# Performance work log

Measured on AMD Instinct MI355X. Metric: run time of the kernel, lower is better.

Reference implementation:

```python
import jax, jax.numpy as jnp
import numpy as np

BOS_TAG_ID = 0
EOS_TAG_ID = 1
NB_FEATURES = 5_000_000
T, L, F_PER = 16384, 64, 14


def setup_inputs() -> dict:
    key = jax.random.key(0)
    k1, k2, k3 = jax.random.split(key, 3)
    feat_idx = jax.random.randint(k1, (T, L, F_PER), 0, NB_FEATURES, dtype=jnp.int64 if jax.config.jax_enable_x64 else jnp.int32)
    emission_weights = jax.random.normal(k2, (NB_FEATURES, 1), dtype=jnp.float32)
    transitions = jax.random.normal(k3, (L, L), dtype=jnp.float32)
    return {"feat_idx": feat_idx, "emission_weights": emission_weights, "transitions": transitions}


def _get_emissions(feat_idx, emission_weights):
    # sparse [L, F] one-hot-count matrix @ [F,1] == gather + sum over the 14 feature ids
    w = emission_weights[:, 0]
    return w[feat_idx].sum(-1)[None]  # [1, T, L]


def _viterbi(emissions, transitions):
    B, T_, L_ = emissions.shape
    alpha0 = transitions[BOS_TAG_ID][None, :] + emissions[:, 0]  # [B, L]

    def step(alpha, em_t):
        # scores[b, prev, cur] = em_t[b, cur] + transitions[prev, cur] + alpha[b, prev]
        scores = em_t[:, None, :] + transitions[None] + alpha[:, :, None]
        new_alpha = scores.max(axis=1)
        bp = scores.argmax(axis=1)  # [B, L]
        return new_alpha, bp

    em_rest = jnp.swapaxes(emissions[:, 1:], 0, 1)  # [T-1, B, L]
    alpha, bps = jax.lax.scan(step, alpha0, em_rest)
    end_scores = alpha + transitions[:, EOS_TAG_ID][None, :]
    max_final_scores = end_scores.max(axis=1)
    final_tags = end_scores.argmax(axis=1)  # [B]

    def back(tag, bp):
        prev = jnp.take_along_axis(bp, tag[:, None], axis=1)[:, 0]
        return prev, prev

    _, path_rest = jax.lax.scan(back, final_tags, bps, reverse=True)  # [T-1, B]
    path = jnp.concatenate([path_rest.T, final_tags[:, None]], axis=1)  # [B, T]
    return max_final_scores, path


def reference(feat_idx, emission_weights, transitions):
    emissions = _get_emissions(feat_idx, emission_weights)
    scores, path = _viterbi(emissions, transitions)
    return scores, path
```

## Files before the change

kernel.cpp:

```cpp
#include <hip/hip_runtime.h>

#define T_LEN  16384
#define LTAG   64
#define F_PER  14
#define NCHUNK 1024
#define CHUNK  16
#define BOS_ID 0
#define EOS_ID 1
#define NREG   6
#define REGSZ  833334
#define WARM   48
#define WB     96

typedef __attribute__((ext_vector_type(4))) int i4;

static constexpr size_t EM_OFF = 0;
static constexpr size_t BP_OFF = EM_OFF + (size_t)T_LEN * 64 * 4;
static constexpr size_t AE_OFF = BP_OFF + (size_t)T_LEN * 64;
static constexpr size_t PS_OFF = AE_OFF + 512;

__global__ __launch_bounds__(256) void k_emissions(
    const int* __restrict__ idx, const float* __restrict__ w, float* __restrict__ em)
{
    __shared__ int sIdx[256 * F_PER];
    const int tid = threadIdx.x;
    const int* g = idx + (size_t)blockIdx.x * (256 * F_PER);
    for (int x = tid * 4; x < 256 * F_PER; x += 1024)
        *(i4*)(sIdx + x) = __builtin_nontemporal_load((const i4*)(g + x));
    __syncthreads();
    int id[F_PER];
#pragma unroll
    for (int f = 0; f < F_PER; ++f) id[f] = sIdx[tid * F_PER + f];
    float sf[F_PER];
#pragma unroll
    for (int f = 0; f < F_PER; ++f) sf[f] = 0.f;
    for (int r = 0; r < NREG; ++r) {
        const int lo = r * REGSZ;
#pragma unroll
        for (int f = 0; f < F_PER; ++f)
            if ((unsigned)(id[f] - lo) < (unsigned)REGSZ) sf[f] += w[id[f]];
    }
    float s = 0.f;
#pragma unroll
    for (int f = 0; f < F_PER; f += 2) s += sf[f] + sf[f + 1];
    em[(size_t)blockIdx.x * 256 + tid] = s;
}

__global__ __launch_bounds__(64, 1) void k_phase3(
    const float* __restrict__ trans, const float* __restrict__ em,
    unsigned char* __restrict__ bp, float* __restrict__ aEnd)
{
    __shared__ __align__(16) float sa[64];
    const int c = blockIdx.x;
    const int tid = threadIdx.x;
    const int t0 = c * CHUNK;
    int nsteps = (T_LEN - 1) - t0; if (nsteps > CHUNK) nsteps = CHUNK;

    float tr_[64];
#pragma unroll
    for (int i = 0; i < 64; ++i) tr_[i] = trans[i * 64 + tid];

    float a; int tw;
    if (t0 <= WARM) { tw = 0; a = tr_[BOS_ID] + em[tid]; }
    else            { tw = t0 - WARM; a = em[(size_t)tw * 64 + tid]; }

    float e_nxt = em[(size_t)(tw + 1) * 64 + tid];
    const float4* ap = (const float4*)sa;

    for (int t = tw + 1; t <= t0; ++t) {
        const float e = e_nxt;
        e_nxt = em[(size_t)(t + 1) * 64 + tid];
        sa[tid] = a;
        float m = -3.0e38f;
#pragma unroll
        for (int g = 0; g < 4; ++g) {
            const float4 v0 = ap[4*g+0], v1 = ap[4*g+1], v2 = ap[4*g+2], v3 = ap[4*g+3];
            float s0[16];
            s0[0]  = tr_[16*g+0]  + v0.x;  s0[1]  = tr_[16*g+1]  + v0.y;
            s0[2]  = tr_[16*g+2]  + v0.z;  s0[3]  = tr_[16*g+3]  + v0.w;
            s0[4]  = tr_[16*g+4]  + v1.x;  s0[5]  = tr_[16*g+5]  + v1.y;
            s0[6]  = tr_[16*g+6]  + v1.z;  s0[7]  = tr_[16*g+7]  + v1.w;
            s0[8]  = tr_[16*g+8]  + v2.x;  s0[9]  = tr_[16*g+9]  + v2.y;
            s0[10] = tr_[16*g+10] + v2.z;  s0[11] = tr_[16*g+11] + v2.w;
            s0[12] = tr_[16*g+12] + v3.x;  s0[13] = tr_[16*g+13] + v3.y;
            s0[14] = tr_[16*g+14] + v3.z;  s0[15] = tr_[16*g+15] + v3.w;
#pragma unroll
            for (int st = 8; st >= 1; st >>= 1)
#pragma unroll
                for (int i = 0; i < st; ++i) s0[i] = fmaxf(s0[i], s0[i + st]);
            m = fmaxf(m, s0[0]);
        }
        a = e + m;
    }

    const int tend = t0 + nsteps;
    for (int t = t0 + 1; t <= tend; ++t) {
        const float e = e_nxt;
        const int tn = (t + 1 <= T_LEN - 1) ? t + 1 : T_LEN - 1;
        e_nxt = em[(size_t)tn * 64 + tid];
        sa[tid] = a;
        float m = -3.0e38f; int bi = 0;
#pragma unroll
        for (int g = 0; g < 4; ++g) {
            const float4 v0 = ap[4*g+0], v1 = ap[4*g+1], v2 = ap[4*g+2], v3 = ap[4*g+3];
            float s0[16];
            s0[0]  = tr_[16*g+0]  + v0.x;  s0[1]  = tr_[16*g+1]  + v0.y;
            s0[2]  = tr_[16*g+2]  + v0.z;  s0[3]  = tr_[16*g+3]  + v0.w;
            s0[4]  = tr_[16*g+4]  + v1.x;  s0[5]  = tr_[16*g+5]  + v1.y;
            s0[6]  = tr_[16*g+6]  + v1.z;  s0[7]  = tr_[16*g+7]  + v1.w;
            s0[8]  = tr_[16*g+8]  + v2.x;  s0[9]  = tr_[16*g+9]  + v2.y;
            s0[10] = tr_[16*g+10] + v2.z;  s0[11] = tr_[16*g+11] + v2.w;
            s0[12] = tr_[16*g+12] + v3.x;  s0[13] = tr_[16*g+13] + v3.y;
            s0[14] = tr_[16*g+14] + v3.z;  s0[15] = tr_[16*g+15] + v3.w;
            float t16[16];
#pragma unroll
            for (int i = 0; i < 16; ++i) t16[i] = s0[i];
#pragma unroll
            for (int st = 8; st >= 1; st >>= 1)
#pragma unroll
                for (int i = 0; i < st; ++i) t16[i] = fmaxf(t16[i], t16[i + st]);
            const float gm = t16[0];
            int gb = 15;
#pragma unroll
            for (int i = 14; i >= 0; --i) gb = (s0[i] == gm) ? i : gb;
            if (gm > m) { m = gm; bi = 16*g + gb; }
        }
        a = e + m;
        bp[(size_t)t * 64 + tid] = (unsigned char)bi;
    }
    if (c == NCHUNK - 1) aEnd[tid] = a;
}

__global__ __launch_bounds__(64) void k_backtrack(
    const float* __restrict__ trans, const float* __restrict__ em,
    const unsigned char* __restrict__ bp, const float* __restrict__ aEnd,
    float* __restrict__ out, double* __restrict__ partial)
{
    __shared__ __align__(16) unsigned char sbp[(CHUNK + WB) * 64];
    const int c = blockIdx.x;
    const int tid = threadIdx.x;
    const int t0 = c * CHUNK;
    int nsteps = (T_LEN - 1) - t0; if (nsteps > CHUNK) nsteps = CHUNK;
    int t_hi = t0 + nsteps + WB; if (t_hi > T_LEN - 1) t_hi = T_LEN - 1;
    const int nrows = t_hi - t0;

    const unsigned char* gsrc = bp + (size_t)(t0 + 1) * 64;
    for (int x = tid * 16; x < nrows * 64; x += 1024)
        *(i4*)(sbp + x) = *(const i4*)(gsrc + x);

    float val = aEnd[tid] + trans[tid * 64 + EOS_ID];
    int idx = tid;
#pragma unroll
    for (int o = 32; o >= 1; o >>= 1) {
        float ov = __shfl_xor(val, o);
        int   oi = __shfl_xor(idx, o);
        if (ov > val || (ov == val && oi < idx)) { val = ov; idx = oi; }
    }
    __syncthreads();

    int tag = (t_hi == T_LEN - 1) ? idx : 0;
    int pp = 0, pt = 0;
    for (int t = t_hi; t > t0; --t) {
        const int r = t - t0;
        if (tid == r)     pp = tag;
        if (tid + 1 == r) pt = tag;
        tag = sbp[(r - 1) * 64 + tag];
    }
    if (tid == 0) pp = tag;

    if (tid < nsteps) out[1 + t0 + tid] = (float)pp;
    if (c == NCHUNK - 1 && tid == nsteps) out[1 + (T_LEN - 1)] = (float)pp;

    double term = 0.0;
    if (tid < nsteps) {
        const int t = t0 + 1 + tid;
        term = (double)trans[pp * 64 + pt] + (double)em[(size_t)t * 64 + pt];
    }
    if (c == 0 && tid == 0)
        term += (double)trans[BOS_ID * 64 + pp] + (double)em[pp];
    if (c == NCHUNK - 1 && tid == nsteps)
        term += (double)trans[pp * 64 + EOS_ID];
#pragma unroll
    for (int o = 1; o < 64; o <<= 1) term += __shfl_xor(term, o);
    if (tid == 0) partial[c] = term;
}

__global__ __launch_bounds__(64) void k_sfin(
    const double* __restrict__ partial, float* __restrict__ out)
{
    const int tid = threadIdx.x;
    double s = 0.0;
    for (int k = tid; k < NCHUNK; k += 64) s += partial[k];
#pragma unroll
    for (int o = 1; o < 64; o <<= 1) s += __shfl_xor(s, o);
    if (tid == 0) out[0] = (float)s;
}

extern "C" void kernel_launch(void* const* d_in, const int* in_sizes, int n_in,
                              void* d_out, int out_size, void* d_ws, size_t ws_size,
                              hipStream_t stream)
{
    const int*   feat = (const int*)d_in[0];
    const float* w    = (const float*)d_in[1];
    const float* tr   = (const float*)d_in[2];
    float* out = (float*)d_out;
    char*  ws  = (char*)d_ws;

    float*         em = (float*)(ws + EM_OFF);
    unsigned char* bp = (unsigned char*)(ws + BP_OFF);
    float*         ae = (float*)(ws + AE_OFF);
    double*        ps = (double*)(ws + PS_OFF);

    k_emissions <<<(T_LEN * LTAG) / 256, 256, 0, stream>>>(feat, w, em);
    k_phase3    <<<NCHUNK, 64, 0, stream>>>(tr, em, bp, ae);
    k_backtrack <<<NCHUNK, 64, 0, stream>>>(tr, em, bp, ae, out, ps);
    k_sfin      <<<1,      64, 0, stream>>>(ps, out);
}
```

Baseline: 226.0 us.

## Double chunk size, deepen emission prefetch, fuse final score reduction via atomics

The chunk length goes from 16 to 32, which halves the number of Viterbi blocks and the redundant warm-up work across chunks, but each block now runs a longer serial recurrence. The emission loads in the forward loop are prefetched two steps ahead instead of one, to hide global load latency. The separate final-sum kernel is removed: each backtrack block adds its partial into a double accumulator with atomics, and a completion counter lets the last block write the score. The accumulator and counter are zeroed in the emissions kernel. Atomic accumulation makes the summation order nondeterministic.

New measurement: 245.3 us. 8.5% more time.

```diff
diff --git a/kernel.cpp b/kernel.cpp
--- a/kernel.cpp
+++ b/kernel.cpp
@@ -3,8 +3,8 @@
 #define T_LEN  16384
 #define LTAG   64
 #define F_PER  14
-#define NCHUNK 1024
-#define CHUNK  16
+#define CHUNK  32
+#define NCHUNK (T_LEN / CHUNK)
 #define BOS_ID 0
 #define EOS_ID 1
 #define NREG   6
@@ -17,13 +17,15 @@
 static constexpr size_t EM_OFF = 0;
 static constexpr size_t BP_OFF = EM_OFF + (size_t)T_LEN * 64 * 4;
 static constexpr size_t AE_OFF = BP_OFF + (size_t)T_LEN * 64;
-static constexpr size_t PS_OFF = AE_OFF + 512;
+static constexpr size_t AC_OFF = AE_OFF + 512;
 
 __global__ __launch_bounds__(256) void k_emissions(
-    const int* __restrict__ idx, const float* __restrict__ w, float* __restrict__ em)
+    const int* __restrict__ idx, const float* __restrict__ w, float* __restrict__ em,
+    double* __restrict__ acc, unsigned int* __restrict__ cnt)
 {
     __shared__ int sIdx[256 * F_PER];
     const int tid = threadIdx.x;
+    if (blockIdx.x == 0 && tid == 0) { *acc = 0.0; *cnt = 0u; }
     const int* g = idx + (size_t)blockIdx.x * (256 * F_PER);
     for (int x = tid * 4; x < 256 * F_PER; x += 1024)
         *(i4*)(sIdx + x) = __builtin_nontemporal_load((const i4*)(g + x));
@@ -65,11 +67,15 @@
     else            { tw = t0 - WARM; a = em[(size_t)tw * 64 + tid]; }
 
     float e_nxt = em[(size_t)(tw + 1) * 64 + tid];
+    int tn2 = tw + 2; if (tn2 > T_LEN - 1) tn2 = T_LEN - 1;
+    float e_nx2 = em[(size_t)tn2 * 64 + tid];
     const float4* ap = (const float4*)sa;
 
     for (int t = tw + 1; t <= t0; ++t) {
         const float e = e_nxt;
-        e_nxt = em[(size_t)(t + 1) * 64 + tid];
+        e_nxt = e_nx2;
+        tn2 = t + 2; if (tn2 > T_LEN - 1) tn2 = T_LEN - 1;
+        e_nx2 = em[(size_t)tn2 * 64 + tid];
         sa[tid] = a;
         float m = -3.0e38f;
 #pragma unroll
@@ -96,8 +102,9 @@
     const int tend = t0 + nsteps;
     for (int t = t0 + 1; t <= tend; ++t) {
         const float e = e_nxt;
-        const int tn = (t + 1 <= T_LEN - 1) ? t + 1 : T_LEN - 1;
-        e_nxt = em[(size_t)tn * 64 + tid];
+        e_nxt = e_nx2;
+        tn2 = t + 2; if (tn2 > T_LEN - 1) tn2 = T_LEN - 1;
+        e_nx2 = em[(size_t)tn2 * 64 + tid];
         sa[tid] = a;
         float m = -3.0e38f; int bi = 0;
 #pragma unroll
@@ -134,7 +141,7 @@
 __global__ __launch_bounds__(64) void k_backtrack(
     const float* __restrict__ trans, const float* __restrict__ em,
     const unsigned char* __restrict__ bp, const float* __restrict__ aEnd,
-    float* __restrict__ out, double* __restrict__ partial)
+    float* __restrict__ out, double* __restrict__ acc, unsigned int* __restrict__ cnt)
 {
     __shared__ __align__(16) unsigned char sbp[(CHUNK + WB) * 64];
     const int c = blockIdx.x;
@@ -182,18 +189,16 @@
         term += (double)trans[pp * 64 + EOS_ID];
 #pragma unroll
     for (int o = 1; o < 64; o <<= 1) term += __shfl_xor(term, o);
-    if (tid == 0) partial[c] = term;
-}
-
-__global__ __launch_bounds__(64) void k_sfin(
-    const double* __restrict__ partial, float* __restrict__ out)
-{
-    const int tid = threadIdx.x;
-    double s = 0.0;
-    for (int k = tid; k < NCHUNK; k += 64) s += partial[k];
-#pragma unroll
-    for (int o = 1; o < 64; o <<= 1) s += __shfl_xor(s, o);
-    if (tid == 0) out[0] = (float)s;
+
+    if (tid == 0) {
+        atomicAdd(acc, term);
+        __threadfence();
+        const unsigned int old = atomicAdd(cnt, 1u);
+        if (old == (unsigned int)(NCHUNK - 1)) {
+            const double tot = atomicAdd(acc, 0.0);
+            out[0] = (float)tot;
+        }
+    }
 }
 
 extern "C" void kernel_launch(void* const* d_in, const int* in_sizes, int n_in,
@@ -206,13 +211,13 @@
     float* out = (float*)d_out;
     char*  ws  = (char*)d_ws;
 
-    float*         em = (float*)(ws + EM_OFF);
-    unsigned char* bp = (unsigned char*)(ws + BP_OFF);
-    float*         ae = (float*)(ws + AE_OFF);
-    double*        ps = (double*)(ws + PS_OFF);
-
-    k_emissions <<<(T_LEN * LTAG) / 256, 256, 0, stream>>>(feat, w, em);
+    float*         em  = (float*)(ws + EM_OFF);
+    unsigned char* bp  = (unsigned char*)(ws + BP_OFF);
+    float*         ae  = (float*)(ws + AE_OFF);
+    double*        acc = (double*)(ws + AC_OFF);
+    unsigned int*  cnt = (unsigned int*)(ws + AC_OFF + 8);
+
+    k_emissions <<<(T_LEN * LTAG) / 256, 256, 0, stream>>>(feat, w, em, acc, cnt);
     k_phase3    <<<NCHUNK, 64, 0, stream>>>(tr, em, bp, ae);
-    k_backtrack <<<NCHUNK, 64, 0, stream>>>(tr, em, bp, ae, out, ps);
-    k_sfin      <<<1,      64, 0, stream>>>(ps, out);
-}
+    k_backtrack <<<NCHUNK, 64, 0, stream>>>(tr, em, bp, ae, out, acc, cnt);
+}
```
